# Performance work log

Hardware: AMD Instinct MI355X
Metric: run time of the kernel (lower is better)

The kernel has to match this reference:

```python
import jax, jax.numpy as jnp
import numpy as np

B, S, D, H = 4, 2048, 1024, 16
HD = D // H  # head_dim = 64


def setup_inputs() -> dict:
    key = jax.random.key(0)
    ks = jax.random.split(key, 11)
    scale = 1.0 / np.sqrt(D)
    return {
        "query": jax.random.normal(ks[0], (B, S, D), jnp.float32),
        "key": jax.random.normal(ks[1], (B, S, D), jnp.float32),
        "value": jax.random.normal(ks[2], (B, S, D), jnp.float32),
        "Wq": jax.random.normal(ks[3], (D, D), jnp.float32) * scale,
        "bq": jnp.zeros((D,), jnp.float32),
        "Wk": jax.random.normal(ks[4], (D, D), jnp.float32) * scale,
        "bk": jnp.zeros((D,), jnp.float32),
        "Wv": jax.random.normal(ks[5], (D, D), jnp.float32) * scale,
        "bv": jnp.zeros((D,), jnp.float32),
        "Wo": jax.random.normal(ks[6], (D, D), jnp.float32) * scale,
        "bo": jnp.zeros((D,), jnp.float32),
    }


def _split_heads(x):
    # [B, S, D] -> [B, H, S, HD]
    return x.reshape(B, -1, H, HD).transpose(0, 2, 1, 3)


def reference(query, key, value, Wq, bq, Wk, bk, Wv, bv, Wo, bo):
    # QKV projections in fp32, then cast to fp16 (faithful to the torch code)
    q = (query @ Wq.T + bq).astype(jnp.float16)
    k = (key @ Wk.T + bk).astype(jnp.float16)
    v = (value @ Wv.T + bv).astype(jnp.float16)
    q, k, v = _split_heads(q), _split_heads(k), _split_heads(v)
    # scores in fp16, scaled by sqrt(head_dim)
    energy = jnp.einsum("bhqd,bhkd->bhqk", q, k) / jnp.float16(np.sqrt(HD))
    attention = jax.nn.softmax(energy, axis=-1)  # fp16 softmax, as in torch
    x = jnp.einsum("bhqk,bhkd->bhqd", attention, v).astype(jnp.float32)
    x = x.transpose(0, 2, 1, 3).reshape(B, -1, D)  # merge heads
    return x @ Wo.T + bo
```

## Files before the change

### kernel.cpp

```cpp
#include <hip/hip_runtime.h>
#include <cstdint>

#define BB 4
#define SS 2048
#define DD 1024
#define HH 16
#define HDIM 64
#define MTOT (BB*SS)

using half_t = _Float16;
typedef _Float16 half2v __attribute__((ext_vector_type(2)));
typedef _Float16 half4v __attribute__((ext_vector_type(4)));
typedef _Float16 half8v __attribute__((ext_vector_type(8)));
typedef float f32x4 __attribute__((ext_vector_type(4)));

#if defined(__has_builtin)
#if __has_builtin(__builtin_amdgcn_exp2f)
#define ATTN_EXP2(x) __builtin_amdgcn_exp2f(x)
#endif
#if __has_builtin(__builtin_amdgcn_cvt_pkrtz)
#define ATTN_PKRTZ 1
#endif
#endif

__device__ __forceinline__ void glds16(const half_t* g, half_t* l) {
    __builtin_amdgcn_global_load_lds(g, l, 16, 0, 0);
}

__global__ __launch_bounds__(256) void split_hi_lo(const float* __restrict__ x,
    half_t* __restrict__ hi, half_t* __restrict__ lo, int n4)
{
    const int i = blockIdx.x * blockDim.x + threadIdx.x;
    if (i >= n4) return;
    float4 v = reinterpret_cast<const float4*>(x)[i];
    float vv[4] = {v.x, v.y, v.z, v.w};
    half4v h, l;
    #pragma unroll
    for (int j = 0; j < 4; ++j) {
        half_t hh = (half_t)vv[j];
        h[j] = hh;
        l[j] = (half_t)(vv[j] - (float)hh);
    }
    reinterpret_cast<half4v*>(hi)[i] = h;
    reinterpret_cast<half4v*>(lo)[i] = l;
}

__global__ __launch_bounds__(256) void cast_w4(
    const float* __restrict__ w0, const float* __restrict__ w1,
    const float* __restrict__ w2, const float* __restrict__ w3,
    half_t* __restrict__ hi)
{
    const int z = blockIdx.z;
    const float* src = z == 0 ? w0 : z == 1 ? w1 : z == 2 ? w2 : w3;
    const size_t base4 = (size_t)z * (DD * DD / 4);
    const size_t i = base4 + blockIdx.x * 256 + threadIdx.x;
    float4 v = reinterpret_cast<const float4*>(src)[blockIdx.x * 256 + threadIdx.x];
    float vv[4] = {v.x, v.y, v.z, v.w};
    half4v h;
    #pragma unroll
    for (int j = 0; j < 4; ++j) h[j] = (half_t)vv[j];
    reinterpret_cast<half4v*>(hi)[i] = h;
}

__global__ __launch_bounds__(256, 4) void gemm_proj(
    const float* __restrict__ A0, const float* __restrict__ A1,
    const float* __restrict__ A2,
    const half_t* __restrict__ WH,
    const float* __restrict__ B0, const float* __restrict__ B1,
    const float* __restrict__ B2,
    half_t* __restrict__ C0, half_t* __restrict__ C1, half_t* __restrict__ C2)
{
    __shared__ __align__(16) half_t AhS[2][128 * 32];
    __shared__ __align__(16) half_t WhS[2][128 * 32];

    const int z = blockIdx.z;
    const float*  A    = z == 0 ? A0 : z == 1 ? A1 : A2;
    const float*  bias = z == 0 ? B0 : z == 1 ? B1 : B2;
    half_t*       C    = z == 0 ? C0 : z == 1 ? C1 : C2;
    const half_t* WHz  = WH + (size_t)z * (DD * DD);

    const int tid = threadIdx.x;
    const int l = tid & 63, w = tid >> 6;
    const int lr = l & 15, lg = l >> 4;
    const int wr = w >> 1, wc = w & 1;
    const int m0 = blockIdx.x * 128, n0 = blockIdx.y * 128;

    const int arow = tid >> 2;
    const int acol = (tid & 3) * 8;
    const int wlrow = l >> 2, wlcol = (l & 3) * 8;

    f32x4 acc[4][4] = {};
    float4 av[2][2];

    #pragma unroll
    for (int j = 0; j < 2; ++j) {
        const float* ap = A + (size_t)(m0 + j * 64 + arow) * DD + acol;
        av[j][0] = *reinterpret_cast<const float4*>(ap);
        av[j][1] = *reinterpret_cast<const float4*>(ap + 4);
    }
    #pragma unroll
    for (int j = 0; j < 2; ++j) {
        half_t hb[8];
        float v0[4] = {av[j][0].x, av[j][0].y, av[j][0].z, av[j][0].w};
        float v1[4] = {av[j][1].x, av[j][1].y, av[j][1].z, av[j][1].w};
        #pragma unroll
        for (int e = 0; e < 4; ++e) { hb[e] = (half_t)v0[e]; hb[4 + e] = (half_t)v1[e]; }
        *reinterpret_cast<int4*>(&AhS[0][(j * 64 + arow) * 32 + acol]) = *reinterpret_cast<int4*>(hb);
    }
    #pragma unroll
    for (int i = 0; i < 2; ++i) {
        const int rr = (w * 2 + i) * 16 + wlrow;
        glds16(WHz + (size_t)(n0 + rr) * DD + wlcol, &WhS[0][(w * 2 + i) * 512]);
    }
    #pragma unroll
    for (int j = 0; j < 2; ++j) {
        const float* ap = A + (size_t)(m0 + j * 64 + arow) * DD + 32 + acol;
        av[j][0] = *reinterpret_cast<const float4*>(ap);
        av[j][1] = *reinterpret_cast<const float4*>(ap + 4);
    }
    __syncthreads();

    for (int t = 0; t < 32; ++t) {
        const int cur = t & 1, nxt = cur ^ 1;
        if (t < 31) {
            const int kk1 = (t + 1) * 32;
            #pragma unroll
            for (int i = 0; i < 2; ++i) {
                const int rr = (w * 2 + i) * 16 + wlrow;
                glds16(WHz + (size_t)(n0 + rr) * DD + kk1 + wlcol, &WhS[nxt][(w * 2 + i) * 512]);
            }
            #pragma unroll
            for (int j = 0; j < 2; ++j) {
                half_t hb[8];
                float v0[4] = {av[j][0].x, av[j][0].y, av[j][0].z, av[j][0].w};
                float v1[4] = {av[j][1].x, av[j][1].y, av[j][1].z, av[j][1].w};
                #pragma unroll
                for (int e = 0; e < 4; ++e) { hb[e] = (half_t)v0[e]; hb[4 + e] = (half_t)v1[e]; }
                *reinterpret_cast<int4*>(&AhS[nxt][(j * 64 + arow) * 32 + acol]) = *reinterpret_cast<int4*>(hb);
            }
        }

        half8v af[4];
        #pragma unroll
        for (int mt = 0; mt < 4; ++mt)
            af[mt] = *reinterpret_cast<const half8v*>(&AhS[cur][(wr * 64 + mt * 16 + lr) * 32 + 8 * lg]);
        #pragma unroll
        for (int nt = 0; nt < 4; ++nt) {
            half8v wf = *reinterpret_cast<const half8v*>(&WhS[cur][(wc * 64 + nt * 16 + lr) * 32 + 8 * lg]);
            #pragma unroll
            for (int mt = 0; mt < 4; ++mt)
                acc[mt][nt] = __builtin_amdgcn_mfma_f32_16x16x32_f16(af[mt], wf, acc[mt][nt], 0, 0, 0);
        }

        if (t < 30) {
            const int kk2 = (t + 2) * 32;
            #pragma unroll
            for (int j = 0; j < 2; ++j) {
                const float* ap = A + (size_t)(m0 + j * 64 + arow) * DD + kk2 + acol;
                av[j][0] = *reinterpret_cast<const float4*>(ap);
                av[j][1] = *reinterpret_cast<const float4*>(ap + 4);
            }
        }
        __syncthreads();
    }

    #pragma unroll
    for (int nt = 0; nt < 4; ++nt) {
        const int n = n0 + wc * 64 + nt * 16 + lr;
        const float bn = bias[n];
        #pragma unroll
        for (int mt = 0; mt < 4; ++mt) {
            const int mbase = m0 + wr * 64 + mt * 16 + 4 * lg;
            #pragma unroll
            for (int j = 0; j < 4; ++j)
                C[(size_t)(mbase + j) * DD + n] = (half_t)(acc[mt][nt][j] + bn);
        }
    }
}

__global__ __launch_bounds__(256, 4) void gemm_out(
    const half_t* __restrict__ Ag,
    const half_t* __restrict__ WHz,
    const float* __restrict__ bias, float* __restrict__ C)
{
    __shared__ __align__(16) half_t AhS[2][128 * 32];
    __shared__ __align__(16) half_t WhS[2][128 * 32];

    const int tid = threadIdx.x;
    const int l = tid & 63, w = tid >> 6;
    const int lr = l & 15, lg = l >> 4;
    const int wr = w >> 1, wc = w & 1;
    const int m0 = blockIdx.x * 128, n0 = blockIdx.y * 128;
    const int wlrow = l >> 2, wlcol = (l & 3) * 8;

    f32x4 acc[4][4] = {};

    #pragma unroll
    for (int i = 0; i < 2; ++i) {
        const int rr = (w * 2 + i) * 16 + wlrow;
        glds16(Ag  + (size_t)(m0 + rr) * DD + wlcol, &AhS[0][(w * 2 + i) * 512]);
        glds16(WHz + (size_t)(n0 + rr) * DD + wlcol, &WhS[0][(w * 2 + i) * 512]);
    }
    __syncthreads();

    for (int t = 0; t < 32; ++t) {
        const int cur = t & 1, nxt = cur ^ 1;
        if (t < 31) {
            const int kk1 = (t + 1) * 32;
            #pragma unroll
            for (int i = 0; i < 2; ++i) {
                const int rr = (w * 2 + i) * 16 + wlrow;
                glds16(Ag  + (size_t)(m0 + rr) * DD + kk1 + wlcol, &AhS[nxt][(w * 2 + i) * 512]);
                glds16(WHz + (size_t)(n0 + rr) * DD + kk1 + wlcol, &WhS[nxt][(w * 2 + i) * 512]);
            }
        }

        half8v af[4];
        #pragma unroll
        for (int mt = 0; mt < 4; ++mt)
            af[mt] = *reinterpret_cast<const half8v*>(&AhS[cur][(wr * 64 + mt * 16 + lr) * 32 + 8 * lg]);
        #pragma unroll
        for (int nt = 0; nt < 4; ++nt) {
            half8v wf = *reinterpret_cast<const half8v*>(&WhS[cur][(wc * 64 + nt * 16 + lr) * 32 + 8 * lg]);
            #pragma unroll
            for (int mt = 0; mt < 4; ++mt)
                acc[mt][nt] = __builtin_amdgcn_mfma_f32_16x16x32_f16(af[mt], wf, acc[mt][nt], 0, 0, 0);
        }
        __syncthreads();
    }

    #pragma unroll
    for (int nt = 0; nt < 4; ++nt) {
        const int n = n0 + wc * 64 + nt * 16 + lr;
        const float bn = bias[n];
        #pragma unroll
        for (int mt = 0; mt < 4; ++mt) {
            const int mbase = m0 + wr * 64 + mt * 16 + 4 * lg;
            #pragma unroll
            for (int j = 0; j < 4; ++j)
                C[(size_t)(mbase + j) * DD + n] = acc[mt][nt][j] + bn;
        }
    }
}

template<int MODE, typename TC>
__global__ __launch_bounds__(256) void gemm3s(
    const half_t* __restrict__ Ah, const half_t* __restrict__ Al,
    const float* __restrict__ Af,
    const half_t* __restrict__ Wh, const half_t* __restrict__ Wl,
    const float* __restrict__ bias, TC* __restrict__ C,
    int Kdim, int Ndim)
{
    constexpr int LDT = 72;
    __shared__ __align__(16) half_t As[128 * LDT];
    __shared__ __align__(16) half_t Ws[128 * LDT];
    const int tid = threadIdx.x;
    const int l = tid & 63, w = tid >> 6;
    const int lr = l & 15, lg = l >> 4;
    const int wr = w >> 1, wc = w & 1;
    const int m0 = blockIdx.y * 128, n0 = blockIdx.x * 128;
    const int r = tid >> 1, t = tid & 1;

    f32x4 acc[4][4] = {};

    for (int kk = 0; kk < Kdim; kk += 32) {
        __syncthreads();
        if constexpr (MODE == 1) {
            const float* ap = Af + (size_t)(m0 + r) * Kdim + kk + 16 * t;
            half_t hbuf[16], lbuf[16];
            #pragma unroll
            for (int u = 0; u < 4; ++u) {
                float4 v = *reinterpret_cast<const float4*>(ap + 4 * u);
                float vv[4] = {v.x, v.y, v.z, v.w};
                #pragma unroll
                for (int j = 0; j < 4; ++j) {
                    half_t hh = (half_t)vv[j];
                    hbuf[4 * u + j] = hh;
                    lbuf[4 * u + j] = (half_t)(vv[j] - (float)hh);
                }
            }
            *reinterpret_cast<int4*>(&As[r * LDT + 16 * t])          = *reinterpret_cast<int4*>(hbuf);
            *reinterpret_cast<int4*>(&As[r * LDT + 16 * t + 8])      = *reinterpret_cast<int4*>(hbuf + 8);
            *reinterpret_cast<int4*>(&As[r * LDT + 40 + 16 * t])     = *reinterpret_cast<int4*>(lbuf);
            *reinterpret_cast<int4*>(&As[r * LDT + 40 + 16 * t + 8]) = *reinterpret_cast<int4*>(lbuf + 8);
        } else {
            const half_t* ap = Ah + (size_t)(m0 + r) * Kdim + kk + 16 * t;
            *reinterpret_cast<int4*>(&As[r * LDT + 16 * t])     = *reinterpret_cast<const int4*>(ap);
            *reinterpret_cast<int4*>(&As[r * LDT + 16 * t + 8]) = *reinterpret_cast<const int4*>(ap + 8);
        }
        {
            const half_t* wp = Wh + (size_t)(n0 + r) * Kdim + kk + 16 * t;
            *reinterpret_cast<int4*>(&Ws[r * LDT + 16 * t])     = *reinterpret_cast<const int4*>(wp);
            *reinterpret_cast<int4*>(&Ws[r * LDT + 16 * t + 8]) = *reinterpret_cast<const int4*>(wp + 8);
            const half_t* wlp = Wl + (size_t)(n0 + r) * Kdim + kk + 16 * t;
            *reinterpret_cast<int4*>(&Ws[r * LDT + 40 + 16 * t])     = *reinterpret_cast<const int4*>(wlp);
            *reinterpret_cast<int4*>(&Ws[r * LDT + 40 + 16 * t + 8]) = *reinterpret_cast<const int4*>(wlp + 8);
        }
        __syncthreads();

        half8v af[4], alf[4];
        #pragma unroll
        for (int mt = 0; mt < 4; ++mt) {
            af[mt] = *reinterpret_cast<const half8v*>(&As[(wr * 64 + mt * 16 + lr) * LDT + 8 * lg]);
            if constexpr (MODE != 2)
                alf[mt] = *reinterpret_cast<const half8v*>(&As[(wr * 64 + mt * 16 + lr) * LDT + 40 + 8 * lg]);
        }
        #pragma unroll
        for (int nt = 0; nt < 4; ++nt) {
            half8v wf  = *reinterpret_cast<const half8v*>(&Ws[(wc * 64 + nt * 16 + lr) * LDT + 8 * lg]);
            half8v wlf = *reinterpret_cast<const half8v*>(&Ws[(wc * 64 + nt * 16 + lr) * LDT + 40 + 8 * lg]);
            #pragma unroll
            for (int mt = 0; mt < 4; ++mt) {
                acc[mt][nt] = __builtin_amdgcn_mfma_f32_16x16x32_f16(af[mt], wf, acc[mt][nt], 0, 0, 0);
                acc[mt][nt] = __builtin_amdgcn_mfma_f32_16x16x32_f16(af[mt], wlf, acc[mt][nt], 0, 0, 0);
                if constexpr (MODE != 2)
                    acc[mt][nt] = __builtin_amdgcn_mfma_f32_16x16x32_f16(alf[mt], wf, acc[mt][nt], 0, 0, 0);
            }
        }
    }

    #pragma unroll
    for (int nt = 0; nt < 4; ++nt) {
        const int n = n0 + wc * 64 + nt * 16 + lr;
        const float bn = bias[n];
        #pragma unroll
        for (int mt = 0; mt < 4; ++mt) {
            const int mbase = m0 + wr * 64 + mt * 16 + 4 * lg;
            #pragma unroll
            for (int j = 0; j < 4; ++j) {
                float v = acc[mt][nt][j] + bn;
                if constexpr (sizeof(TC) == 4)
                    C[(size_t)(mbase + j) * Ndim + n] = v;
                else
                    C[(size_t)(mbase + j) * Ndim + n] = (half_t)v;
            }
        }
    }
}

template<typename TA, typename TC>
__global__ __launch_bounds__(256) void gemm_bias(const TA* __restrict__ A,
    const float* __restrict__ W, const float* __restrict__ bias,
    TC* __restrict__ C, int Mdim, int Ndim, int Kdim)
{
    constexpr int BK = 16;
    __shared__ float As[BK][68];
    __shared__ float Ws[BK][68];
    const int tx = threadIdx.x, ty = threadIdx.y;
    const int tid = ty * 16 + tx;
    const int m0 = blockIdx.y * 64, n0 = blockIdx.x * 64;
    const int lrow = tid >> 2;
    const int lc4  = (tid & 3) * 4;

    float acc[4][4] = {};
    for (int kk = 0; kk < Kdim; kk += BK) {
        {
            const TA* ap = A + (size_t)(m0 + lrow) * Kdim + kk + lc4;
            float a0, a1, a2, a3;
            if constexpr (sizeof(TA) == 4) {
                float4 v = *reinterpret_cast<const float4*>(ap);
                a0 = v.x; a1 = v.y; a2 = v.z; a3 = v.w;
            } else {
                half2v v0 = *reinterpret_cast<const half2v*>(ap);
                half2v v1 = *reinterpret_cast<const half2v*>(ap + 2);
                a0 = (float)v0[0]; a1 = (float)v0[1];
                a2 = (float)v1[0]; a3 = (float)v1[1];
            }
            As[lc4 + 0][lrow] = a0; As[lc4 + 1][lrow] = a1;
            As[lc4 + 2][lrow] = a2; As[lc4 + 3][lrow] = a3;
            const float* wp = W + (size_t)(n0 + lrow) * Kdim + kk + lc4;
            float4 wv = *reinterpret_cast<const float4*>(wp);
            Ws[lc4 + 0][lrow] = wv.x; Ws[lc4 + 1][lrow] = wv.y;
            Ws[lc4 + 2][lrow] = wv.z; Ws[lc4 + 3][lrow] = wv.w;
        }
        __syncthreads();
        #pragma unroll
        for (int k = 0; k < BK; ++k) {
            float4 av = *reinterpret_cast<const float4*>(&As[k][ty * 4]);
            float4 bv = *reinterpret_cast<const float4*>(&Ws[k][tx * 4]);
            float a[4] = {av.x, av.y, av.z, av.w};
            float b[4] = {bv.x, bv.y, bv.z, bv.w};
            #pragma unroll
            for (int i = 0; i < 4; ++i)
                #pragma unroll
                for (int j = 0; j < 4; ++j)
                    acc[i][j] = fmaf(a[i], b[j], acc[i][j]);
        }
        __syncthreads();
    }
    #pragma unroll
    for (int i = 0; i < 4; ++i) {
        const int m = m0 + ty * 4 + i;
        #pragma unroll
        for (int j = 0; j < 4; ++j) {
            const int n = n0 + tx * 4 + j;
            float v = acc[i][j] + bias[n];
            if constexpr (sizeof(TC) == 4)
                C[(size_t)m * Ndim + n] = v;
            else
                C[(size_t)m * Ndim + n] = (half_t)v;
        }
    }
}

__global__ __launch_bounds__(256, 4) void attn_fused(const half_t* __restrict__ Q,
    const half_t* __restrict__ K, const half_t* __restrict__ V,
    half_t* __restrict__ X)
{
    __shared__ __align__(16) half_t KsL[2][64 * 64];
    __shared__ __align__(16) half_t Vt[2][64 * 72];

    const int tid = threadIdx.x;
    const int l   = tid & 63;
    const int w   = tid >> 6;
    const int lr  = l & 15;
    const int lg  = l >> 4;

    const int phys = blockIdx.x;
    const int virt = (phys & 7) * 128 + (phys >> 3);
    const int qb = virt & 15;
    const int h  = (virt >> 4) & 15;
    const int b  = virt >> 8;

    const int q0 = qb * 128 + w * 32;
    const size_t hoff = (size_t)(b * SS) * DD + h * HDIM;

    half8v qf[2][2];
    #pragma unroll
    for (int s = 0; s < 2; ++s) {
        const half_t* qp = Q + hoff + (size_t)(q0 + s * 16 + lr) * DD;
        #pragma unroll
        for (int hb = 0; hb < 2; ++hb) {
            half8v v = *reinterpret_cast<const half8v*>(qp + hb * 32 + 8 * lg);
            #pragma unroll
            for (int e = 0; e < 8; ++e) v[e] *= (half_t)0.125f;
            qf[s][hb] = v;
        }
    }

    int koffH[2];
    #pragma unroll
    for (int i = 0; i < 2; ++i) {
        const int R    = (w * 2 + i) * 8 + (l >> 3);
        const int gkey = ((R >> 5) & 1) * 32 + ((R >> 2) & 3) * 8
                       + ((R >> 4) & 1) * 4 + (R & 3);
        const int gc   = (l & 7) ^ (R & 7);
        koffH[i] = gkey * DD + gc * 8;
    }
    const int kidx0 = lr * 64 + ((lg ^ (lr & 7)) * 8);
    const int kidx1 = lr * 64 + (((4 + lg) ^ (lr & 7)) * 8);

    const int vk2 = tid & 31, vdq = tid >> 5;

    float m[2]    = {-1e30f, -1e30f};
    float lsum[2] = {0.f, 0.f};
    f32x4 xacc[2][4] = {};

    half4v va0, va1, vb0, vb1;
    {
        const half_t* kbase = K + hoff;
        glds16(kbase + koffH[0], &KsL[0][(w * 2 + 0) * 512]);
        glds16(kbase + koffH[1], &KsL[0][(w * 2 + 1) * 512]);
        const half_t* vsrc = V + hoff + (size_t)(2 * vk2) * DD + vdq * 8;
        va0 = *reinterpret_cast<const half4v*>(vsrc);
        va1 = *reinterpret_cast<const half4v*>(vsrc + 4);
        vb0 = *reinterpret_cast<const half4v*>(vsrc + DD);
        vb1 = *reinterpret_cast<const half4v*>(vsrc + DD + 4);
        #pragma unroll
        for (int i = 0; i < 4; ++i) {
            half2v p0 = {va0[i], vb0[i]};
            half2v p1 = {va1[i], vb1[i]};
            *reinterpret_cast<half2v*>(&Vt[0][(vdq * 8 + i) * 72 + 2 * vk2])     = p0;
            *reinterpret_cast<half2v*>(&Vt[0][(vdq * 8 + i + 4) * 72 + 2 * vk2]) = p1;
        }
    }
    __syncthreads();

    for (int t = 0; t < SS / 64; ++t) {
        const int cur = t & 1, nxt = cur ^ 1;
        if (t < SS / 64 - 1) {
            const half_t* kbase = K + hoff + (size_t)(t + 1) * 64 * DD;
            glds16(kbase + koffH[0], &KsL[nxt][(w * 2 + 0) * 512]);
            glds16(kbase + koffH[1], &KsL[nxt][(w * 2 + 1) * 512]);
            const half_t* vsrc = V + hoff + (size_t)((t + 1) * 64 + 2 * vk2) * DD + vdq * 8;
            va0 = *reinterpret_cast<const half4v*>(vsrc);
            va1 = *reinterpret_cast<const half4v*>(vsrc + 4);
            vb0 = *reinterpret_cast<const half4v*>(vsrc + DD);
            vb1 = *reinterpret_cast<const half4v*>(vsrc + DD + 4);
        }

        half8v kf[4][2];
        #pragma unroll
        for (int kb = 0; kb < 4; ++kb) {
            kf[kb][0] = *reinterpret_cast<const half8v*>(&KsL[cur][kb * 1024 + kidx0]);
            kf[kb][1] = *reinterpret_cast<const half8v*>(&KsL[cur][kb * 1024 + kidx1]);
        }

        half8v af2[2][2];
        #pragma unroll
        for (int s = 0; s < 2; ++s) {
            f32x4 c[4] = {};
            __builtin_amdgcn_s_setprio(1);
            #pragma unroll
            for (int kb = 0; kb < 4; ++kb)
                #pragma unroll
                for (int hb = 0; hb < 2; ++hb)
                    c[kb] = __builtin_amdgcn_mfma_f32_16x16x32_f16(kf[kb][hb], qf[s][hb], c[kb], 0, 0, 0);
            __builtin_amdgcn_s_setprio(0);

            float r0 = fmaxf(fmaxf(c[0][0], c[0][1]), fmaxf(c[0][2], c[0][3]));
            float r1 = fmaxf(fmaxf(c[1][0], c[1][1]), fmaxf(c[1][2], c[1][3]));
            float r2 = fmaxf(fmaxf(c[2][0], c[2][1]), fmaxf(c[2][2], c[2][3]));
            float r3 = fmaxf(fmaxf(c[3][0], c[3][1]), fmaxf(c[3][2], c[3][3]));
            float rmax = fmaxf(fmaxf(r0, r1), fmaxf(r2, r3));
            rmax = fmaxf(rmax, __shfl_xor(rmax, 16, 64));
            rmax = fmaxf(rmax, __shfl_xor(rmax, 32, 64));

            if (__any(rmax > m[s] + 8.0f)) {
                const float mn = fmaxf(m[s], rmax);
                const float sc = __expf(m[s] - mn);
                lsum[s] *= sc;
                #pragma unroll
                for (int db = 0; db < 4; ++db)
                    #pragma unroll
                    for (int j = 0; j < 4; ++j)
                        xacc[s][db][j] *= sc;
                m[s] = mn;
            }

            const float L2E = 1.4426950408889634f;
            const float nm2 = m[s] * -L2E;
            float ps = 0.f;
            #pragma unroll
            for (int kb = 0; kb < 4; ++kb) {
#ifdef ATTN_EXP2
                const float p0 = ATTN_EXP2(__builtin_fmaf(c[kb][0], L2E, nm2));
                const float p1 = ATTN_EXP2(__builtin_fmaf(c[kb][1], L2E, nm2));
                const float p2 = ATTN_EXP2(__builtin_fmaf(c[kb][2], L2E, nm2));
                const float p3 = ATTN_EXP2(__builtin_fmaf(c[kb][3], L2E, nm2));
#else
                const float p0 = __expf(c[kb][0] - m[s]);
                const float p1 = __expf(c[kb][1] - m[s]);
                const float p2 = __expf(c[kb][2] - m[s]);
                const float p3 = __expf(c[kb][3] - m[s]);
#endif
                ps += (p0 + p1) + (p2 + p3);
#ifdef ATTN_PKRTZ
                auto lo = __builtin_amdgcn_cvt_pkrtz(p0, p1);
                auto hi = __builtin_amdgcn_cvt_pkrtz(p2, p3);
                af2[s][kb >> 1][(kb & 1) * 4 + 0] = (half_t)lo[0];
                af2[s][kb >> 1][(kb & 1) * 4 + 1] = (half_t)lo[1];
                af2[s][kb >> 1][(kb & 1) * 4 + 2] = (half_t)hi[0];
                af2[s][kb >> 1][(kb & 1) * 4 + 3] = (half_t)hi[1];
#else
                af2[s][kb >> 1][(kb & 1) * 4 + 0] = (half_t)p0;
                af2[s][kb >> 1][(kb & 1) * 4 + 1] = (half_t)p1;
                af2[s][kb >> 1][(kb & 1) * 4 + 2] = (half_t)p2;
                af2[s][kb >> 1][(kb & 1) * 4 + 3] = (half_t)p3;
#endif
            }
            ps += __shfl_xor(ps, 16, 64);
            ps += __shfl_xor(ps, 32, 64);
            lsum[s] += ps;
        }

        __builtin_amdgcn_s_setprio(1);
        #pragma unroll
        for (int db = 0; db < 4; ++db)
            #pragma unroll
            for (int kb2 = 0; kb2 < 2; ++kb2) {
                half8v vf = *reinterpret_cast<const half8v*>(
                    &Vt[cur][(db * 16 + lr) * 72 + kb2 * 32 + 8 * lg]);
                xacc[0][db] = __builtin_amdgcn_mfma_f32_16x16x32_f16(vf, af2[0][kb2], xacc[0][db], 0, 0, 0);
                xacc[1][db] = __builtin_amdgcn_mfma_f32_16x16x32_f16(vf, af2[1][kb2], xacc[1][db], 0, 0, 0);
            }
        __builtin_amdgcn_s_setprio(0);

        if (t < SS / 64 - 1) {
            #pragma unroll
            for (int i = 0; i < 4; ++i) {
                half2v p0 = {va0[i], vb0[i]};
                half2v p1 = {va1[i], vb1[i]};
                *reinterpret_cast<half2v*>(&Vt[nxt][(vdq * 8 + i) * 72 + 2 * vk2])     = p0;
                *reinterpret_cast<half2v*>(&Vt[nxt][(vdq * 8 + i + 4) * 72 + 2 * vk2]) = p1;
            }
        }
        __syncthreads();
    }

    #pragma unroll
    for (int s = 0; s < 2; ++s) {
        const float invl = 1.0f / lsum[s];
        half_t* xp = X + hoff + (size_t)(q0 + s * 16 + lr) * DD;
        #pragma unroll
        for (int db = 0; db < 4; ++db) {
            half4v o;
            #pragma unroll
            for (int j = 0; j < 4; ++j) o[j] = (half_t)(xacc[s][db][j] * invl);
            *reinterpret_cast<half4v*>(xp + db * 16 + 4 * lg) = o;
        }
    }
}

extern "C" void kernel_launch(void* const* d_in, const int* in_sizes, int n_in,
                              void* d_out, int out_size, void* d_ws, size_t ws_size,
                              hipStream_t stream) {
    const float* q   = (const float*)d_in[0];
    const float* k   = (const float*)d_in[1];
    const float* v   = (const float*)d_in[2];
    const float* Wq  = (const float*)d_in[3];
    const float* bq  = (const float*)d_in[4];
    const float* Wk  = (const float*)d_in[5];
    const float* bk  = (const float*)d_in[6];
    const float* Wv  = (const float*)d_in[7];
    const float* bv  = (const float*)d_in[8];
    const float* Wo  = (const float*)d_in[9];
    const float* bo  = (const float*)d_in[10];
    float* out = (float*)d_out;

    const size_t MB = 1ull << 20;
    const size_t ACT = (size_t)MTOT * DD;
    const size_t WEL = (size_t)DD * DD;

    half_t* q16 = (half_t*)d_ws;
    half_t* k16 = q16 + ACT;
    half_t* v16 = k16 + ACT;
    half_t* x16 = v16 + ACT;

    dim3 gblk(256);
    dim3 ablk(256);
    dim3 agrd(1024);

    if (ws_size >= 76 * MB) {
        half_t* wh = x16 + ACT;

        dim3 wsgrd(WEL / 4 / 256, 1, 4);
        hipLaunchKernelGGL(cast_w4, wsgrd, gblk, 0, stream,
                           Wq, Wk, Wv, Wo, wh);

        dim3 pgrd(MTOT / 128, DD / 128, 3);
        hipLaunchKernelGGL(gemm_proj, pgrd, gblk, 0, stream,
                           q, k, v, wh, bq, bk, bv, q16, k16, v16);

        hipLaunchKernelGGL(attn_fused, agrd, ablk, 0, stream, q16, k16, v16, x16);

        dim3 ogrd(MTOT / 128, DD / 128);
        hipLaunchKernelGGL(gemm_out, ogrd, gblk, 0, stream,
                           x16, wh + 3 * WEL, bo, out);
    } else if (ws_size >= 72 * MB) {
        half_t* wh = x16 + ACT;
        half_t* wl = wh + WEL;
        const int nw4 = (int)(WEL / 4);
        dim3 sgW((nw4 + 255) / 256);
        dim3 ggrd(DD / 128, MTOT / 128);

        hipLaunchKernelGGL(split_hi_lo, sgW, gblk, 0, stream, Wq, wh, wl, nw4);
        hipLaunchKernelGGL((gemm3s<1, half_t>), ggrd, gblk, 0, stream,
                           nullptr, nullptr, q, wh, wl, bq, q16, DD, DD);
        hipLaunchKernelGGL(split_hi_lo, sgW, gblk, 0, stream, Wk, wh, wl, nw4);
        hipLaunchKernelGGL((gemm3s<1, half_t>), ggrd, gblk, 0, stream,
                           nullptr, nullptr, k, wh, wl, bk, k16, DD, DD);
        hipLaunchKernelGGL(split_hi_lo, sgW, gblk, 0, stream, Wv, wh, wl, nw4);
        hipLaunchKernelGGL((gemm3s<1, half_t>), ggrd, gblk, 0, stream,
                           nullptr, nullptr, v, wh, wl, bv, v16, DD, DD);

        hipLaunchKernelGGL(attn_fused, agrd, ablk, 0, stream, q16, k16, v16, x16);

        hipLaunchKernelGGL(split_hi_lo, sgW, gblk, 0, stream, Wo, wh, wl, nw4);
        hipLaunchKernelGGL((gemm3s<2, float>), ggrd, gblk, 0, stream,
                           x16, nullptr, nullptr, wh, wl, bo, out, DD, DD);
    } else {
        dim3 blk(16, 16);
        dim3 grd(DD / 64, MTOT / 64);
        hipLaunchKernelGGL((gemm_bias<float, half_t>), grd, blk, 0, stream,
                           q, Wq, bq, q16, MTOT, DD, DD);
        hipLaunchKernelGGL((gemm_bias<float, half_t>), grd, blk, 0, stream,
                           k, Wk, bk, k16, MTOT, DD, DD);
        hipLaunchKernelGGL((gemm_bias<float, half_t>), grd, blk, 0, stream,
                           v, Wv, bv, v16, MTOT, DD, DD);
        hipLaunchKernelGGL(attn_fused, agrd, ablk, 0, stream, q16, k16, v16, x16);
        hipLaunchKernelGGL((gemm_bias<half_t, float>), grd, blk, 0, stream,
                           x16, Wo, bo, out, MTOT, DD, DD);
    }
}
```

Before: 211.9 us.

## Pre-cast fp32 activations to fp16 and load projection A tiles directly to LDS

```diff
diff --git a/kernel.cpp b/kernel.cpp
--- a/kernel.cpp
+++ b/kernel.cpp
@@ -62,9 +62,26 @@
     reinterpret_cast<half4v*>(hi)[i] = h;
 }
 
-__global__ __launch_bounds__(256, 4) void gemm_proj(
-    const float* __restrict__ A0, const float* __restrict__ A1,
-    const float* __restrict__ A2,
+__global__ __launch_bounds__(256) void cast_a3(
+    const float* __restrict__ a0, const float* __restrict__ a1,
+    const float* __restrict__ a2,
+    half_t* __restrict__ d0, half_t* __restrict__ d1, half_t* __restrict__ d2)
+{
+    const int z = blockIdx.z;
+    const float* src = z == 0 ? a0 : z == 1 ? a1 : a2;
+    half_t*      dst = z == 0 ? d0 : z == 1 ? d1 : d2;
+    const size_t i = (size_t)blockIdx.x * 256 + threadIdx.x;
+    float4 v = reinterpret_cast<const float4*>(src)[i];
+    float vv[4] = {v.x, v.y, v.z, v.w};
+    half4v h;
+    #pragma unroll
+    for (int j = 0; j < 4; ++j) h[j] = (half_t)vv[j];
+    reinterpret_cast<half4v*>(dst)[i] = h;
+}
+
+__global__ __launch_bounds__(256, 5) void gemm_projf(
+    const half_t* __restrict__ A0, const half_t* __restrict__ A1,
+    const half_t* __restrict__ A2,
     const half_t* __restrict__ WH,
     const float* __restrict__ B0, const float* __restrict__ B1,
     const float* __restrict__ B2,
@@ -74,7 +91,7 @@
     __shared__ __align__(16) half_t WhS[2][128 * 32];
 
     const int z = blockIdx.z;
-    const float*  A    = z == 0 ? A0 : z == 1 ? A1 : A2;
+    const half_t* A    = z == 0 ? A0 : z == 1 ? A1 : A2;
     const float*  bias = z == 0 ? B0 : z == 1 ? B1 : B2;
     half_t*       C    = z == 0 ? C0 : z == 1 ? C1 : C2;
     const half_t* WHz  = WH + (size_t)z * (DD * DD);
@@ -84,39 +101,15 @@
     const int lr = l & 15, lg = l >> 4;
     const int wr = w >> 1, wc = w & 1;
     const int m0 = blockIdx.x * 128, n0 = blockIdx.y * 128;
-
-    const int arow = tid >> 2;
-    const int acol = (tid & 3) * 8;
     const int wlrow = l >> 2, wlcol = (l & 3) * 8;
 
     f32x4 acc[4][4] = {};
-    float4 av[2][2];
-
-    #pragma unroll
-    for (int j = 0; j < 2; ++j) {
-        const float* ap = A + (size_t)(m0 + j * 64 + arow) * DD + acol;
-        av[j][0] = *reinterpret_cast<const float4*>(ap);
-        av[j][1] = *reinterpret_cast<const float4*>(ap + 4);
-    }
-    #pragma unroll
-    for (int j = 0; j < 2; ++j) {
-        half_t hb[8];
-        float v0[4] = {av[j][0].x, av[j][0].y, av[j][0].z, av[j][0].w};
-        float v1[4] = {av[j][1].x, av[j][1].y, av[j][1].z, av[j][1].w};
-        #pragma unroll
-        for (int e = 0; e < 4; ++e) { hb[e] = (half_t)v0[e]; hb[4 + e] = (half_t)v1[e]; }
-        *reinterpret_cast<int4*>(&AhS[0][(j * 64 + arow) * 32 + acol]) = *reinterpret_cast<int4*>(hb);
-    }
+
     #pragma unroll
     for (int i = 0; i < 2; ++i) {
         const int rr = (w * 2 + i) * 16 + wlrow;
+        glds16(A   + (size_t)(m0 + rr) * DD + wlcol, &AhS[0][(w * 2 + i) * 512]);
         glds16(WHz + (size_t)(n0 + rr) * DD + wlcol, &WhS[0][(w * 2 + i) * 512]);
-    }
-    #pragma unroll
-    for (int j = 0; j < 2; ++j) {
-        const float* ap = A + (size_t)(m0 + j * 64 + arow) * DD + 32 + acol;
-        av[j][0] = *reinterpret_cast<const float4*>(ap);
-        av[j][1] = *reinterpret_cast<const float4*>(ap + 4);
     }
     __syncthreads();
 
@@ -127,16 +120,8 @@
             #pragma unroll
             for (int i = 0; i < 2; ++i) {
                 const int rr = (w * 2 + i) * 16 + wlrow;
+                glds16(A   + (size_t)(m0 + rr) * DD + kk1 + wlcol, &AhS[nxt][(w * 2 + i) * 512]);
                 glds16(WHz + (size_t)(n0 + rr) * DD + kk1 + wlcol, &WhS[nxt][(w * 2 + i) * 512]);
-            }
-            #pragma unroll
-            for (int j = 0; j < 2; ++j) {
-                half_t hb[8];
-                float v0[4] = {av[j][0].x, av[j][0].y, av[j][0].z, av[j][0].w};
-                float v1[4] = {av[j][1].x, av[j][1].y, av[j][1].z, av[j][1].w};
-                #pragma unroll
-                for (int e = 0; e < 4; ++e) { hb[e] = (half_t)v0[e]; hb[4 + e] = (half_t)v1[e]; }
-                *reinterpret_cast<int4*>(&AhS[nxt][(j * 64 + arow) * 32 + acol]) = *reinterpret_cast<int4*>(hb);
             }
         }
 
@@ -150,16 +135,6 @@
             #pragma unroll
             for (int mt = 0; mt < 4; ++mt)
                 acc[mt][nt] = __builtin_amdgcn_mfma_f32_16x16x32_f16(af[mt], wf, acc[mt][nt], 0, 0, 0);
-        }
-
-        if (t < 30) {
-            const int kk2 = (t + 2) * 32;
-            #pragma unroll
-            for (int j = 0; j < 2; ++j) {
-                const float* ap = A + (size_t)(m0 + j * 64 + arow) * DD + kk2 + acol;
-                av[j][0] = *reinterpret_cast<const float4*>(ap);
-                av[j][1] = *reinterpret_cast<const float4*>(ap + 4);
-            }
         }
         __syncthreads();
     }
@@ -178,7 +153,7 @@
     }
 }
 
-__global__ __launch_bounds__(256, 4) void gemm_out(
+__global__ __launch_bounds__(256, 5) void gemm_out(
     const half_t* __restrict__ Ag,
     const half_t* __restrict__ WHz,
     const float* __restrict__ bias, float* __restrict__ C)
@@ -633,14 +608,21 @@
 
     if (ws_size >= 76 * MB) {
         half_t* wh = x16 + ACT;
+        half_t* qa = (half_t*)d_out;
+        half_t* ka = qa + ACT;
+        half_t* va = x16;
 
         dim3 wsgrd(WEL / 4 / 256, 1, 4);
         hipLaunchKernelGGL(cast_w4, wsgrd, gblk, 0, stream,
                            Wq, Wk, Wv, Wo, wh);
 
+        dim3 asgrd(ACT / 4 / 256, 1, 3);
+        hipLaunchKernelGGL(cast_a3, asgrd, gblk, 0, stream,
+                           q, k, v, qa, ka, va);
+
         dim3 pgrd(MTOT / 128, DD / 128, 3);
-        hipLaunchKernelGGL(gemm_proj, pgrd, gblk, 0, stream,
-                           q, k, v, wh, bq, bk, bv, q16, k16, v16);
+        hipLaunchKernelGGL(gemm_projf, pgrd, gblk, 0, stream,
+                           qa, ka, va, wh, bq, bk, bv, q16, k16, v16);
 
         hipLaunchKernelGGL(attn_fused, agrd, ablk, 0, stream, q16, k16, v16, x16);
 
```

After: 246.7 us. 1.16x slower.
